# Performance work log

Measured on AMD Instinct MI355X. Metric: run time of the kernel, lower is better.

## Reference

```python
import jax, jax.numpy as jnp
import numpy as np

TEMPERATURE = 0.5
EPS = 1e-8          # torch CosineSimilarity denominator clamp
NEG_INF = -1e30     # finite stand-in for -inf padding (grad-safe)


def setup_inputs() -> dict:
    key = jax.random.key(0)
    k1, k2, k3 = jax.random.split(key, 3)
    B, D = 4096, 256
    z_i = jax.random.normal(k1, (B, D), dtype=jnp.float32)
    z_j = jax.random.normal(k2, (B, D), dtype=jnp.float32)
    labels = jax.random.randint(k3, (B,), 0, 100, dtype=jnp.int64)
    return {"z_i": z_i, "z_j": z_j, "labels": labels}


def reference(z_i, z_j, labels):
    B = z_i.shape[0]
    z = jnp.concatenate([z_i, z_j], axis=0)          # [N, D], N = 2B
    lab = jnp.concatenate([labels, labels], axis=0)  # [N]
    N = 2 * B

    # cosine similarity matrix / temperature
    norm = jnp.maximum(jnp.linalg.norm(z, axis=1, keepdims=True), EPS)
    zn = z / norm                                    # [N, D]
    sim = (zn @ zn.T) / TEMPERATURE                  # [N, N]

    # positives: sim[i, i+B] and sim[i+B, i]
    pos = jnp.concatenate(
        [jnp.diagonal(sim, offset=B), jnp.diagonal(sim, offset=-B)], axis=0
    )                                                # [N]

    # negatives mask: different label (diagonal & positive pair share a label,
    # so torch's explicit zeroing of them is already implied by label inequality)
    mask = lab[:, None] != lab[None, :]              # [N, N] bool

    # CE with target index 0 over [pos | padded negatives]:
    # loss_i = logsumexp(pos_i, negs_i) - pos_i  (padding -inf is a no-op in lse)
    neg_logits = jnp.where(mask, sim, NEG_INF)       # [N, N]
    row_max = jnp.maximum(pos, jnp.max(neg_logits, axis=1))          # [N]
    lse = row_max + jnp.log(
        jnp.exp(pos - row_max)
        + jnp.sum(jnp.exp(neg_logits - row_max[:, None]), axis=1)
    )                                                # [N]
    loss = jnp.sum(lse - pos) / N
    return loss
```

## Files before the change

### kernel.cpp

```cpp
#include <hip/hip_runtime.h>
#include <hip/hip_bf16.h>


#define B_ 4096
#define N_ 8192
#define D_ 256
#define EPS_ 1e-8f
#define SPLITS 16
#define BM 128
#define BN 32
#define KC 8
#define CPS (N_ / SPLITS)
#define NT_ (CPS / BN)
#define LOG2E 1.44269504088896340736f

typedef __attribute__((ext_vector_type(8))) short bfrag_t;
typedef __attribute__((ext_vector_type(4))) float f32x4_t;

__device__ __forceinline__ ushort f2bf_rne(float x) {
  union { float f; unsigned u; } a; a.f = x;
  unsigned r = a.u + 0x7FFFu + ((a.u >> 16) & 1u);
  return (ushort)(r >> 16);
}

__device__ __forceinline__ void cp16_lds(const uint4* g, uint4* l) {
  __builtin_amdgcn_global_load_lds(
      (const __attribute__((address_space(1))) unsigned int*)g,
      (__attribute__((address_space(3))) unsigned int*)l, 16, 0, 0);
}

__global__ __launch_bounds__(256) void k_prep(
    const float* __restrict__ zi, const float* __restrict__ zj,
    ushort* __restrict__ zn, float* __restrict__ pos) {
  const int w = threadIdx.x >> 6, lane = threadIdx.x & 63;
  const int p = blockIdx.x * 4 + w;
  float4 a = reinterpret_cast<const float4*>(zi + (size_t)p * D_)[lane];
  float4 b = reinterpret_cast<const float4*>(zj + (size_t)p * D_)[lane];
  float si = a.x * a.x + a.y * a.y + a.z * a.z + a.w * a.w;
  float sj = b.x * b.x + b.y * b.y + b.z * b.z + b.w * b.w;
  float dd = a.x * b.x + a.y * b.y + a.z * b.z + a.w * b.w;
#pragma unroll
  for (int d = 1; d < 64; d <<= 1) {
    si += __shfl_xor(si, d);
    sj += __shfl_xor(sj, d);
    dd += __shfl_xor(dd, d);
  }
  const float ni = fmaxf(sqrtf(si), EPS_), nj = fmaxf(sqrtf(sj), EPS_);
  const float ii = 1.0f / ni, ij = 1.0f / nj;
  ushort4 oi, oj;
  oi.x = f2bf_rne(a.x * ii); oi.y = f2bf_rne(a.y * ii);
  oi.z = f2bf_rne(a.z * ii); oi.w = f2bf_rne(a.w * ii);
  oj.x = f2bf_rne(b.x * ij); oj.y = f2bf_rne(b.y * ij);
  oj.z = f2bf_rne(b.z * ij); oj.w = f2bf_rne(b.w * ij);
  reinterpret_cast<ushort4*>(zn + (size_t)p * D_)[lane] = oi;
  reinterpret_cast<ushort4*>(zn + (size_t)(p + B_) * D_)[lane] = oj;
  if (lane == 0) {
    float v = dd / (ni * nj) * 2.0f;
    pos[p] = v;
    pos[p + B_] = v;
  }
}

__global__ __launch_bounds__(256, 4) void k_flash(
    const ushort* __restrict__ zn, const int* __restrict__ labels,
    float* __restrict__ Spart) {
  __shared__ uint4 lds16[2 * BN * 32];
  __shared__ int labbuf[CPS];
  const int tid = threadIdx.x;
  const int w = tid >> 6, lane = tid & 63;
  const int l15 = lane & 15, l4 = lane >> 4;
  const int c31 = lane & 31, lh = lane >> 5;

  const int bid = blockIdx.x;
  const int swz = (bid & 7) * 128 + (bid >> 3);
  const int rowblk = swz & 63, split = swz >> 6;
  const int arowb = rowblk * BM + w * 32;

  bfrag_t a[2][KC];
#pragma unroll
  for (int mf = 0; mf < 2; ++mf) {
    const int ar = arowb + mf * 16 + l15;
#pragma unroll
    for (int kc = 0; kc < KC; ++kc)
      a[mf][kc] = *reinterpret_cast<const bfrag_t*>(
          zn + (size_t)ar * D_ + kc * 32 + l4 * 8);
  }

  labbuf[tid]       = labels[(split * CPS + tid) & (B_ - 1)];
  labbuf[tid + 256] = labels[(split * CPS + tid + 256) & (B_ - 1)];

  int labR[2][4];
#pragma unroll
  for (int mf = 0; mf < 2; ++mf)
#pragma unroll
    for (int rg = 0; rg < 4; ++rg)
      labR[mf][rg] = labels[(arowb + mf * 16 + l4 * 4 + rg) & (B_ - 1)];

  float Srun[2][4];
#pragma unroll
  for (int mf = 0; mf < 2; ++mf)
#pragma unroll
    for (int rg = 0; rg < 4; ++rg) Srun[mf][rg] = 0.f;

  const int offp0 = l15 * 512 + ((l4 ^ (l15 & 7)) << 4);
  const int offp1 = l15 * 512 + (((4 + l4) ^ (l15 & 7)) << 4);
  uint so[4];
#pragma unroll
  for (int q = 0; q < 4; ++q) {
    const int rw = w * 8 + q * 2 + lh;
    so[q] = rw * 32 + (c31 ^ (rw & 7));
  }
  const uint4* gsplit =
      reinterpret_cast<const uint4*>(zn) + (size_t)(split * CPS) * 32;

  auto stage = [&](int t) {
    const uint4* gt = gsplit + t * (BN * 32);
    uint4* db = lds16 + ((t & 1) * (BN * 32)) + w * 256;
#pragma unroll
    for (int q = 0; q < 4; ++q) cp16_lds(gt + so[q], db + q * 64);
  };

  stage(0);
  __syncthreads();

#pragma unroll 2
  for (int ct = 0; ct < NT_; ++ct) {
    if (ct + 1 < NT_) stage(ct + 1);

    int labC[2];
#pragma unroll
    for (int nf = 0; nf < 2; ++nf)
      labC[nf] = labbuf[ct * BN + nf * 16 + l15];

    f32x4_t acc[2][2];
#pragma unroll
    for (int mf = 0; mf < 2; ++mf)
#pragma unroll
      for (int nf = 0; nf < 2; ++nf)
        acc[mf][nf] = (f32x4_t){0.f, 0.f, 0.f, 0.f};

    const char* lb = (const char*)lds16 + ((ct & 1) << 14);
#pragma unroll
    for (int kc = 0; kc < KC; ++kc) {
      const int kimm = (kc >> 1) << 7;
      const int po = (kc & 1) ? offp1 : offp0;
#pragma unroll
      for (int nf = 0; nf < 2; ++nf) {
        bfrag_t bf = *reinterpret_cast<const bfrag_t*>(
            lb + po + nf * 8192 + kimm);
        acc[0][nf] = __builtin_amdgcn_mfma_f32_16x16x32_bf16(a[0][kc], bf, acc[0][nf], 0, 0, 0);
        acc[1][nf] = __builtin_amdgcn_mfma_f32_16x16x32_bf16(a[1][kc], bf, acc[1][nf], 0, 0, 0);
      }
    }

#pragma unroll
    for (int mf = 0; mf < 2; ++mf) {
#pragma unroll
      for (int rg = 0; rg < 4; ++rg) {
        const int rl = labR[mf][rg];
        float e0, e1;
        {
          float t0 = fmaf(acc[mf][0][rg], 2.0f * LOG2E, -2.0f * LOG2E);
          e0 = __builtin_amdgcn_exp2f(t0);
          e0 = (labC[0] != rl) ? e0 : 0.0f;
        }
        {
          float t1 = fmaf(acc[mf][1][rg], 2.0f * LOG2E, -2.0f * LOG2E);
          e1 = __builtin_amdgcn_exp2f(t1);
          e1 = (labC[1] != rl) ? e1 : 0.0f;
        }
        Srun[mf][rg] += e0 + e1;
      }
    }

    __syncthreads();
  }

#pragma unroll
  for (int mf = 0; mf < 2; ++mf) {
#pragma unroll
    for (int rg = 0; rg < 4; ++rg) {
      float s = Srun[mf][rg];
#pragma unroll
      for (int d = 1; d < 16; d <<= 1) s += __shfl_xor(s, d);
      if (l15 == 0)
        Spart[(size_t)split * N_ + arowb + mf * 16 + l4 * 4 + rg] = s;
    }
  }
}

__global__ __launch_bounds__(1024) void k_finalize(
    const float* __restrict__ Spart, const float* __restrict__ pos,
    float* __restrict__ out) {
  __shared__ float red[16];
  const int tid = threadIdx.x;
  float c = 0.f;
#pragma unroll
  for (int k = 0; k < 8; ++k) {
    const int i = k * 1024 + tid;
    const float p = pos[i];
    float S = __builtin_amdgcn_exp2f(fmaf(p, LOG2E, -2.0f * LOG2E));
#pragma unroll
    for (int s = 0; s < SPLITS; ++s) S += Spart[s * N_ + i];
    c += 2.0f + __logf(S) - p;
  }
#pragma unroll
  for (int d = 1; d < 64; d <<= 1) c += __shfl_xor(c, d);
  if ((tid & 63) == 0) red[tid >> 6] = c;
  __syncthreads();
  if (tid == 0) {
    float t = 0.f;
#pragma unroll
    for (int q = 0; q < 16; ++q) t += red[q];
    out[0] = t * (1.0f / (float)N_);
  }
}

extern "C" void kernel_launch(void* const* d_in, const int* in_sizes, int n_in,
                              void* d_out, int out_size, void* d_ws, size_t ws_size,
                              hipStream_t stream) {
  (void)in_sizes; (void)n_in; (void)out_size; (void)ws_size;
  const float* zi = (const float*)d_in[0];
  const float* zj = (const float*)d_in[1];
  const int* labels = (const int*)d_in[2];
  char* ws = (char*)d_ws;
  ushort* zn   = (ushort*)(ws);
  float* pos   = (float*)(ws + 4u * 1024 * 1024);
  float* Spart = (float*)(ws + 4u * 1024 * 1024 + 32 * 1024);
  float* out = (float*)d_out;

  k_prep<<<B_ / 4, 256, 0, stream>>>(zi, zj, zn, pos);
  k_flash<<<(N_ / BM) * SPLITS, 256, 0, stream>>>(zn, labels, Spart);
  k_finalize<<<1, 1024, 0, stream>>>(Spart, pos, out);
}
```

Baseline: 111.7 us.

## Software-pipeline MFMA with exp epilogue and parallelize finalize reduction

Restructures the flash loop into a two-tile ping-pong so each tile's MFMA runs while the previous tile's exp/mask epilogue is computed, using two accumulator sets. Separately, the single-block finalize becomes a multi-block kernel that accumulates into the output via atomicAdd, with the output zeroed in the prep kernel. This adds register pressure from the second accumulator set and makes the final sum order nondeterministic.

```diff
diff --git a/kernel.cpp b/kernel.cpp
--- a/kernel.cpp
+++ b/kernel.cpp
@@ -31,7 +31,8 @@
 
 __global__ __launch_bounds__(256) void k_prep(
     const float* __restrict__ zi, const float* __restrict__ zj,
-    ushort* __restrict__ zn, float* __restrict__ pos) {
+    ushort* __restrict__ zn, float* __restrict__ pos, float* __restrict__ out) {
+  if (blockIdx.x == 0 && threadIdx.x == 0) out[0] = 0.0f;
   const int w = threadIdx.x >> 6, lane = threadIdx.x & 63;
   const int p = blockIdx.x * 4 + w;
   float4 a = reinterpret_cast<const float4*>(zi + (size_t)p * D_)[lane];
@@ -112,69 +113,77 @@
   }
   const uint4* gsplit =
       reinterpret_cast<const uint4*>(zn) + (size_t)(split * CPS) * 32;
-
-  auto stage = [&](int t) {
+  const char* lb0 = (const char*)lds16;
+  const char* lb1 = (const char*)lds16 + (1 << 14);
+
+  auto stage = [&](int t, int bufsel) {
     const uint4* gt = gsplit + t * (BN * 32);
-    uint4* db = lds16 + ((t & 1) * (BN * 32)) + w * 256;
+    uint4* db = lds16 + bufsel * (BN * 32) + w * 256;
 #pragma unroll
     for (int q = 0; q < 4; ++q) cp16_lds(gt + so[q], db + q * 64);
   };
 
-  stage(0);
-  __syncthreads();
-
-#pragma unroll 2
-  for (int ct = 0; ct < NT_; ++ct) {
-    if (ct + 1 < NT_) stage(ct + 1);
-
-    int labC[2];
-#pragma unroll
-    for (int nf = 0; nf < 2; ++nf)
-      labC[nf] = labbuf[ct * BN + nf * 16 + l15];
-
-    f32x4_t acc[2][2];
+  auto mfma_tile = [&](const char* lb, f32x4_t (&acc)[2][2]) {
 #pragma unroll
     for (int mf = 0; mf < 2; ++mf)
 #pragma unroll
       for (int nf = 0; nf < 2; ++nf)
         acc[mf][nf] = (f32x4_t){0.f, 0.f, 0.f, 0.f};
-
-    const char* lb = (const char*)lds16 + ((ct & 1) << 14);
 #pragma unroll
     for (int kc = 0; kc < KC; ++kc) {
       const int kimm = (kc >> 1) << 7;
       const int po = (kc & 1) ? offp1 : offp0;
 #pragma unroll
       for (int nf = 0; nf < 2; ++nf) {
-        bfrag_t bf = *reinterpret_cast<const bfrag_t*>(
-            lb + po + nf * 8192 + kimm);
+        bfrag_t bf = *reinterpret_cast<const bfrag_t*>(lb + po + nf * 8192 + kimm);
         acc[0][nf] = __builtin_amdgcn_mfma_f32_16x16x32_bf16(a[0][kc], bf, acc[0][nf], 0, 0, 0);
         acc[1][nf] = __builtin_amdgcn_mfma_f32_16x16x32_bf16(a[1][kc], bf, acc[1][nf], 0, 0, 0);
       }
     }
-
+  };
+
+  auto epi = [&](int ct, f32x4_t (&acc)[2][2]) {
+    const int lc0 = labbuf[ct * BN + l15];
+    const int lc1 = labbuf[ct * BN + 16 + l15];
 #pragma unroll
     for (int mf = 0; mf < 2; ++mf) {
 #pragma unroll
       for (int rg = 0; rg < 4; ++rg) {
         const int rl = labR[mf][rg];
-        float e0, e1;
-        {
-          float t0 = fmaf(acc[mf][0][rg], 2.0f * LOG2E, -2.0f * LOG2E);
-          e0 = __builtin_amdgcn_exp2f(t0);
-          e0 = (labC[0] != rl) ? e0 : 0.0f;
-        }
-        {
-          float t1 = fmaf(acc[mf][1][rg], 2.0f * LOG2E, -2.0f * LOG2E);
-          e1 = __builtin_amdgcn_exp2f(t1);
-          e1 = (labC[1] != rl) ? e1 : 0.0f;
-        }
+        float t0 = fmaf(acc[mf][0][rg], 2.0f * LOG2E, -2.0f * LOG2E);
+        float t1 = fmaf(acc[mf][1][rg], 2.0f * LOG2E, -2.0f * LOG2E);
+        float e0 = __builtin_amdgcn_exp2f(t0);
+        float e1 = __builtin_amdgcn_exp2f(t1);
+        e0 = (lc0 != rl) ? e0 : 0.0f;
+        e1 = (lc1 != rl) ? e1 : 0.0f;
         Srun[mf][rg] += e0 + e1;
       }
     }
-
+  };
+
+  f32x4_t accA[2][2], accB[2][2];
+
+  stage(0, 0);
+  __syncthreads();
+  stage(1, 1);
+  mfma_tile(lb0, accA);
+  __syncthreads();
+
+#pragma unroll
+  for (int c2 = 0; c2 < (NT_ - 2) / 2; ++c2) {
+    const int ct = 1 + 2 * c2;
+    stage(ct + 1, 0);
+    mfma_tile(lb1, accB);
+    epi(ct - 1, accA);
     __syncthreads();
-  }
+    stage(ct + 2, 1);
+    mfma_tile(lb0, accA);
+    epi(ct, accB);
+    __syncthreads();
+  }
+  mfma_tile(lb1, accB);
+  epi(NT_ - 2, accA);
+  epi(NT_ - 1, accB);
 
 #pragma unroll
   for (int mf = 0; mf < 2; ++mf) {
@@ -189,30 +198,24 @@
   }
 }
 
-__global__ __launch_bounds__(1024) void k_finalize(
+__global__ __launch_bounds__(256) void k_finalize(
     const float* __restrict__ Spart, const float* __restrict__ pos,
     float* __restrict__ out) {
-  __shared__ float red[16];
-  const int tid = threadIdx.x;
-  float c = 0.f;
-#pragma unroll
-  for (int k = 0; k < 8; ++k) {
-    const int i = k * 1024 + tid;
-    const float p = pos[i];
-    float S = __builtin_amdgcn_exp2f(fmaf(p, LOG2E, -2.0f * LOG2E));
-#pragma unroll
-    for (int s = 0; s < SPLITS; ++s) S += Spart[s * N_ + i];
-    c += 2.0f + __logf(S) - p;
-  }
+  __shared__ float red[4];
+  const int i = blockIdx.x * 256 + threadIdx.x;
+  const float p = pos[i];
+  float S = __builtin_amdgcn_exp2f(fmaf(p, LOG2E, -2.0f * LOG2E));
+#pragma unroll
+  for (int s = 0; s < SPLITS; ++s) S += Spart[s * N_ + i];
+  float c = 2.0f + __logf(S) - p;
 #pragma unroll
   for (int d = 1; d < 64; d <<= 1) c += __shfl_xor(c, d);
-  if ((tid & 63) == 0) red[tid >> 6] = c;
+  const int w = threadIdx.x >> 6, lane = threadIdx.x & 63;
+  if (lane == 0) red[w] = c;
   __syncthreads();
-  if (tid == 0) {
-    float t = 0.f;
-#pragma unroll
-    for (int q = 0; q < 16; ++q) t += red[q];
-    out[0] = t * (1.0f / (float)N_);
+  if (threadIdx.x == 0) {
+    float t = red[0] + red[1] + red[2] + red[3];
+    atomicAdd(out, t * (1.0f / (float)N_));
   }
 }
 
@@ -229,7 +232,7 @@
   float* Spart = (float*)(ws + 4u * 1024 * 1024 + 32 * 1024);
   float* out = (float*)d_out;
 
-  k_prep<<<B_ / 4, 256, 0, stream>>>(zi, zj, zn, pos);
+  k_prep<<<B_ / 4, 256, 0, stream>>>(zi, zj, zn, pos, out);
   k_flash<<<(N_ / BM) * SPLITS, 256, 0, stream>>>(zn, labels, Spart);
-  k_finalize<<<1, 1024, 0, stream>>>(Spart, pos, out);
-}
+  k_finalize<<<N_ / 256, 256, 0, stream>>>(Spart, pos, out);
+}
```

Result: slower. 332.9 us (+198.1%).
